# Performance work log

Measured on AMD Instinct MI355X. Metric: run time of the kernel, lower is better.

The kernel has to match this reference:

```python
import jax, jax.numpy as jnp
import numpy as np

B, S, D, H, M = 2, 2048, 1024, 16, 40
DH = D // H  # 64
L = S + M    # kv length after memory concat


def setup_inputs() -> dict:
    key = jax.random.key(0)
    ks = jax.random.split(key, 20)
    s = 1.0 / np.sqrt(D)
    inp = {
        'v': jax.random.normal(ks[0], (B, S, D), jnp.float32),
        'k': jax.random.normal(ks[1], (B, S, D), jnp.float32),
        'q': jax.random.normal(ks[2], (B, S, D), jnp.float32),
        # additive binary mask (1 = masked out), broadcast over heads
        'mask': jax.random.randint(ks[3], (B, 1, S, L), 0, 2).astype(jnp.float32),
        'Wq': jax.random.normal(ks[4], (D, D), jnp.float32) * s,
        'bq': jnp.zeros((D,), jnp.float32),
        'Wk': jax.random.normal(ks[5], (D, D), jnp.float32) * s,
        'bk': jnp.zeros((D,), jnp.float32),
        'Wv': jax.random.normal(ks[6], (D, D), jnp.float32) * s,
        'bv': jnp.zeros((D,), jnp.float32),
        'k_memory': jax.random.normal(ks[7], (1, M, D), jnp.float32) * (1.0 / np.sqrt(DH)),
        'v_memory': jax.random.normal(ks[8], (1, M, D), jnp.float32) * (1.0 / np.sqrt(M)),
        'Wkm': jax.random.normal(ks[9], (D, D), jnp.float32) * s,
        'bkm': jnp.zeros((D,), jnp.float32),
        'Wvm': jax.random.normal(ks[10], (D, D), jnp.float32) * s,
        'bvm': jnp.zeros((D,), jnp.float32),
        'Wo': jax.random.normal(ks[11], (D, D), jnp.float32) * s,
        'bo': jnp.zeros((D,), jnp.float32),
    }
    return inp


def _split_heads(x):
    # [B, T, D] -> [B, H, T, DH]
    b, t, _ = x.shape
    return x.reshape(b, t, H, DH).transpose(0, 2, 1, 3)


def reference(v, k, q, mask, Wq, bq, Wk, bk, Wv, bv, k_memory, v_memory,
              Wkm, bkm, Wvm, bvm, Wo, bo):
    qp = q @ Wq + bq
    kp = k @ Wk + bk
    vp = v @ Wv + bv
    km = (k_memory @ Wkm + bkm)  # [1, M, D]
    vm = (v_memory @ Wvm + bvm)  # [1, M, D]
    kc = jnp.concatenate([kp, jnp.broadcast_to(km, (kp.shape[0], M, D))], axis=1)
    vc = jnp.concatenate([vp, jnp.broadcast_to(vm, (vp.shape[0], M, D))], axis=1)
    qh, kh, vh = _split_heads(qp), _split_heads(kc), _split_heads(vc)
    # scores: [B, H, S, L]
    scores = jnp.einsum('bhqd,bhkd->bhqk', qh, kh) / np.sqrt(DH)
    scores = scores + mask * (-1e9)
    attn = jax.nn.softmax(scores, axis=-1)
    ctx = jnp.einsum('bhqk,bhkd->bhqd', attn, vh)  # [B, H, S, DH]
    ctx = ctx.transpose(0, 2, 1, 3).reshape(ctx.shape[0], S, D)
    out = ctx @ Wo + bo
    return (out, attn)
```

## Files before the change

### kernel.cpp

```cpp
#include <hip/hip_runtime.h>
#include <hip/hip_bf16.h>

typedef __attribute__((ext_vector_type(8))) short short8v;
typedef __attribute__((ext_vector_type(4))) short short4v;
typedef __attribute__((ext_vector_type(4))) float f32x4;

constexpr int B_ = 2, S_ = 2048, H_ = 16, MM_ = 40;
constexpr int L_ = S_ + MM_;
constexpr int LP_ = 2112;
constexpr int NT_ = 33;
constexpr float QSCALE = 0.18033688011112042f;

struct S2 { short hi, lo; };
__device__ __forceinline__ S2 split2(float f) {
    unsigned u = __builtin_bit_cast(unsigned, f);
    short hi = (short)(u >> 16);
    float fh = __builtin_bit_cast(float, u & 0xFFFF0000u);
    float fl = f - fh;
    short lo = (short)(__builtin_bit_cast(unsigned, fl) >> 16);
    return {hi, lo};
}
__device__ __forceinline__ short f2bh(float f) {
    unsigned u = __builtin_bit_cast(unsigned, f);
    u = (u + 0x7FFFu + ((u >> 16) & 1u)) >> 16;
    return (short)u;
}
__device__ __forceinline__ f32x4 mfma16(short8v a, short8v b, f32x4 c) {
    return __builtin_amdgcn_mfma_f32_16x16x32_bf16(a, b, c, 0, 0, 0);
}
__device__ __forceinline__ unsigned cvt_pk_bf16(float a, float b) {
    unsigned r;
    asm("v_cvt_pk_bf16_f32 %0, %1, %2" : "=v"(r) : "v"(a), "v"(b));
    return r;
}

__global__ __launch_bounds__(256) void wsplit6_kernel(
    const float* __restrict__ W0, const float* __restrict__ W1,
    const float* __restrict__ W2, const float* __restrict__ W3,
    const float* __restrict__ W4, const float* __restrict__ W5,
    short* __restrict__ WT)
{
    const float* Ws[6] = {W0, W1, W2, W3, W4, W5};
    const float* W = Ws[blockIdx.z];
    short* WTh = WT + (size_t)blockIdx.z * 2097152;
    short* WTl = WTh + 1048576;
    __shared__ float T[64][68];
    const int t = threadIdx.x;
    const int k0 = blockIdx.x * 64, n0 = blockIdx.y * 64;
    {
        int r = t >> 2, c = (t & 3) * 16;
        const float* src = W + (size_t)(k0 + r) * 1024 + n0 + c;
        *(float4*)&T[r][c + 0]  = *(const float4*)(src + 0);
        *(float4*)&T[r][c + 4]  = *(const float4*)(src + 4);
        *(float4*)&T[r][c + 8]  = *(const float4*)(src + 8);
        *(float4*)&T[r][c + 12] = *(const float4*)(src + 12);
    }
    __syncthreads();
    {
        int n = t >> 2, ks = (t & 3) * 16;
        short8v h0, h1, l0, l1;
#pragma unroll
        for (int j = 0; j < 8; ++j) {
            S2 a = split2(T[ks + j][n]);     h0[j] = a.hi; l0[j] = a.lo;
            S2 b = split2(T[ks + 8 + j][n]); h1[j] = b.hi; l1[j] = b.lo;
        }
        size_t dst = (size_t)(n0 + n) * 1024 + k0 + ks;
        *(short8v*)(WTh + dst) = h0;  *(short8v*)(WTh + dst + 8) = h1;
        *(short8v*)(WTl + dst) = l0;  *(short8v*)(WTl + dst + 8) = l1;
    }
}

__global__ __launch_bounds__(256) void pad_clear(short* __restrict__ Vh)
{
    int idx = blockIdx.x * 256 + threadIdx.x;
    if (idx >= 2048 * 24) return;
    int rd = idx / 24, l = L_ + idx % 24;
    Vh[(size_t)rd * LP_ + l] = 0;
}

template<int ASRC>
__device__ __forceinline__ void gemm_core(
    const float* __restrict__ Af, const short* __restrict__ Ahg,
    const short* __restrict__ Alg, const short* __restrict__ WTh,
    const short* __restrict__ WTl, const float* __restrict__ bias,
    float bscale, float scale,
    short* __restrict__ Oh, short* __restrict__ Ol, float* __restrict__ Of,
    int M, int RPB, int TD, int loff, int omode, int bx, int by,
    int kbeg, int kend)
{
    __shared__ short Ah[128][40];
    __shared__ short Al[128][40];
    __shared__ short Bh[128][40];
    __shared__ short Bl[128][40];
    const int tid = threadIdx.x;
    const int lane = tid & 63, wid = tid >> 6;
    const int wr = wid >> 1, wc = wid & 1;
    const int row0 = by * 128, col0 = bx * 128;
    const int sr = tid >> 1, sc = (tid & 1) << 4;

    f32x4 acc[4][4] = {};

    for (int k0 = kbeg; k0 < kend; k0 += 32) {
        if (ASRC == 0) {
            float f[16];
            int gr = row0 + sr;
            if (gr < M) {
                const float* ap = Af + (size_t)gr * 1024 + k0 + sc;
                float4 a0 = *(const float4*)(ap + 0);
                float4 a1 = *(const float4*)(ap + 4);
                float4 a2 = *(const float4*)(ap + 8);
                float4 a3 = *(const float4*)(ap + 12);
                f[0]=a0.x; f[1]=a0.y; f[2]=a0.z; f[3]=a0.w;
                f[4]=a1.x; f[5]=a1.y; f[6]=a1.z; f[7]=a1.w;
                f[8]=a2.x; f[9]=a2.y; f[10]=a2.z; f[11]=a2.w;
                f[12]=a3.x; f[13]=a3.y; f[14]=a3.z; f[15]=a3.w;
            } else {
#pragma unroll
                for (int j = 0; j < 16; ++j) f[j] = 0.f;
            }
            short8v h0, h1, l0, l1;
#pragma unroll
            for (int j = 0; j < 8; ++j) {
                S2 s = split2(f[j]); h0[j] = s.hi; l0[j] = s.lo;
            }
#pragma unroll
            for (int j = 0; j < 8; ++j) {
                S2 s = split2(f[8 + j]); h1[j] = s.hi; l1[j] = s.lo;
            }
            *(short8v*)&Ah[sr][sc] = h0; *(short8v*)&Ah[sr][sc + 8] = h1;
            *(short8v*)&Al[sr][sc] = l0; *(short8v*)&Al[sr][sc + 8] = l1;
        } else {
            const short* ah = Ahg + (size_t)(row0 + sr) * 1024 + k0 + sc;
            const short* al = Alg + (size_t)(row0 + sr) * 1024 + k0 + sc;
            *(short8v*)&Ah[sr][sc]     = *(const short8v*)ah;
            *(short8v*)&Ah[sr][sc + 8] = *(const short8v*)(ah + 8);
            *(short8v*)&Al[sr][sc]     = *(const short8v*)al;
            *(short8v*)&Al[sr][sc + 8] = *(const short8v*)(al + 8);
        }
        {
            const short* bh = WTh + (size_t)(col0 + sr) * 1024 + k0 + sc;
            const short* bl = WTl + (size_t)(col0 + sr) * 1024 + k0 + sc;
            *(short8v*)&Bh[sr][sc]     = *(const short8v*)bh;
            *(short8v*)&Bh[sr][sc + 8] = *(const short8v*)(bh + 8);
            *(short8v*)&Bl[sr][sc]     = *(const short8v*)bl;
            *(short8v*)&Bl[sr][sc + 8] = *(const short8v*)(bl + 8);
        }
        __syncthreads();
        const int kof = (lane >> 4) << 3;
        const int ar = lane & 15;
        short8v afh[4], afl[4], bfh[4], bfl[4];
#pragma unroll
        for (int i = 0; i < 4; ++i) {
            afh[i] = *(const short8v*)&Ah[wr * 64 + i * 16 + ar][kof];
            afl[i] = *(const short8v*)&Al[wr * 64 + i * 16 + ar][kof];
            bfh[i] = *(const short8v*)&Bh[wc * 64 + i * 16 + ar][kof];
            bfl[i] = *(const short8v*)&Bl[wc * 64 + i * 16 + ar][kof];
        }
#pragma unroll
        for (int i = 0; i < 4; ++i)
#pragma unroll
            for (int j = 0; j < 4; ++j) {
                acc[i][j] = mfma16(afh[i], bfh[j], acc[i][j]);
                acc[i][j] = mfma16(afh[i], bfl[j], acc[i][j]);
                acc[i][j] = mfma16(afl[i], bfh[j], acc[i][j]);
            }
        __syncthreads();
    }

#pragma unroll
    for (int i = 0; i < 4; ++i) {
#pragma unroll
        for (int j = 0; j < 4; ++j) {
            int colb = col0 + wc * 64 + j * 16 + (lane & 15);
            float bv = bias[colb] * bscale;
            int rowb = row0 + wr * 64 + i * 16 + ((lane >> 4) << 2);
            if (omode == 2) {
                if (rowb < M) {
                    int bb = rowb / RPB, tt = rowb % RPB;
                    int hh = colb >> 6, dh = colb & 63;
                    short4v hs;
#pragma unroll
                    for (int r = 0; r < 4; ++r)
                        hs[r] = f2bh((acc[i][j][r] + bv) * scale);
                    size_t dst = ((size_t)(bb * H_ + hh) * 64 + dh) * LP_ + loff + tt;
                    *(short4v*)(Oh + dst) = hs;
                }
            } else {
#pragma unroll
                for (int r = 0; r < 4; ++r) {
                    int row = rowb + r;
                    if (row < M) {
                        float o = (acc[i][j][r] + bv) * scale;
                        int bb = row / RPB, tt = row % RPB;
                        if (omode == 0) {
                            Of[((size_t)bb * TD + loff + tt) * 1024 + colb] = o;
                        } else {
                            int hh = colb >> 6, dh = colb & 63;
                            size_t dst = ((size_t)(bb * H_ + hh) * TD + loff + tt) * 64 + dh;
                            S2 s = split2(o);
                            Oh[dst] = s.hi; Ol[dst] = s.lo;
                        }
                    }
                }
            }
        }
    }
}

__global__ __launch_bounds__(256) void qkv_gemm(
    const float* __restrict__ q_in, const float* __restrict__ k_in,
    const float* __restrict__ v_in, const short* __restrict__ WT,
    const float* __restrict__ bq, const float* __restrict__ bk,
    const float* __restrict__ bv,
    short* __restrict__ Qh, short* __restrict__ Ql,
    short* __restrict__ Kh, short* __restrict__ Kl, short* __restrict__ Vh,
    const float* __restrict__ mask, unsigned* __restrict__ mp)
{
    const int z = blockIdx.z;
    if (z == 3) {
        const int blk = blockIdx.y * 8 + blockIdx.x;
        for (int rr = 0; rr < 16; ++rr) {
            const int row = blk * 16 + rr;
            const float* mr = mask + (size_t)row * L_;
            unsigned* orow = mp + (size_t)row * 68;
            for (int wd = threadIdx.x; wd < 66; wd += 256) {
                int l0 = wd * 32;
                unsigned bits = 0u;
                int lim = (wd < 65) ? 32 : 8;
                for (int j = 0; j < lim; j += 4) {
                    float4 m4 = *(const float4*)(mr + l0 + j);
                    bits |= ((unsigned)(m4.x != 0.f)) << (j + 0);
                    bits |= ((unsigned)(m4.y != 0.f)) << (j + 1);
                    bits |= ((unsigned)(m4.z != 0.f)) << (j + 2);
                    bits |= ((unsigned)(m4.w != 0.f)) << (j + 3);
                }
                if (wd == 65) bits |= 0xFFFFFF00u;
                orow[wd] = bits;
            }
        }
        return;
    }
    const float* A = (z == 0) ? q_in : (z == 1) ? k_in : v_in;
    const short* WTh = WT + (size_t)z * 2097152;
    const short* WTl = WTh + 1048576;
    const float* bias = (z == 0) ? bq : (z == 1) ? bk : bv;
    float scale = (z == 0) ? QSCALE : 1.0f;
    short* Oh = (z == 0) ? Qh : (z == 1) ? Kh : Vh;
    short* Ol = (z == 0) ? Ql : Kl;
    int omode = (z == 2) ? 2 : 1;
    int TD = (z == 0) ? S_ : LP_;
    gemm_core<0>(A, nullptr, nullptr, WTh, WTl, bias, 1.0f, scale,
                 Oh, Ol, nullptr, 4096, 2048, TD, 0, omode,
                 blockIdx.x, blockIdx.y, 0, 1024);
}

__global__ __launch_bounds__(256) void mem_gemm(
    const float* __restrict__ kmem, const float* __restrict__ vmem,
    const short* __restrict__ WT,
    const float* __restrict__ bkm, const float* __restrict__ bvm,
    short* __restrict__ Kh, short* __restrict__ Kl, short* __restrict__ Vh)
{
    const int z = blockIdx.z;
    const int which = z >> 1, b = z & 1;
    const float* A = which ? vmem : kmem;
    const short* WTh = WT + (size_t)(3 + which) * 2097152;
    const short* WTl = WTh + 1048576;
    const float* bias = which ? bvm : bkm;
    short* Oh = which ? (Vh + (size_t)b * H_ * 64 * LP_)
                      : (Kh + (size_t)b * H_ * LP_ * 64);
    short* Ol = which ? nullptr : (Kl + (size_t)b * H_ * LP_ * 64);
    gemm_core<0>(A, nullptr, nullptr, WTh, WTl, bias, 1.0f, 1.0f,
                 Oh, Ol, nullptr, 40, 40, LP_, S_, which ? 2 : 1,
                 blockIdx.x, blockIdx.y, 0, 1024);
}

__global__ __launch_bounds__(256) void out_gemm(
    const short* __restrict__ Ch, const short* __restrict__ Cl,
    const short* __restrict__ WT, const float* __restrict__ bo,
    float* __restrict__ Po0, float* __restrict__ Po1)
{
    const int z = blockIdx.z;
    const short* WTh = WT + (size_t)5 * 2097152;
    gemm_core<1>(nullptr, Ch, Cl, WTh, WTh + 1048576, bo,
                 z == 0 ? 1.0f : 0.0f, 1.0f,
                 nullptr, nullptr, z == 0 ? Po0 : Po1, 4096, 2048, S_, 0, 0,
                 blockIdx.x, blockIdx.y, z * 512, z * 512 + 512);
}

__global__ __launch_bounds__(256) void add_out(
    const float* __restrict__ Po0, const float* __restrict__ Po1,
    float* __restrict__ outp)
{
    int i = (blockIdx.x * 256 + threadIdx.x) * 4;
    float4 a = *(const float4*)(Po0 + i);
    float4 b = *(const float4*)(Po1 + i);
    a.x += b.x; a.y += b.y; a.z += b.z; a.w += b.w;
    *(float4*)(outp + i) = a;
}

__global__ __launch_bounds__(256) void attn4_kernel(
    const short* __restrict__ Qh, const short* __restrict__ Ql,
    const short* __restrict__ Kh, const short* __restrict__ Kl,
    const short* __restrict__ Vh, const unsigned* __restrict__ mp,
    float* __restrict__ attn, float* __restrict__ invg,
    short* __restrict__ Ch, short* __restrict__ Cl)
{
    __shared__ short KhB[2][64][64];
    __shared__ short KlB[2][64][64];
    __shared__ short VB[64][64];
    __shared__ short Ph[4][16][68];
    __shared__ float sbuf[4][16];

    const int id = blockIdx.x;
    const int wg = (id & 7) * 128 + (id >> 3);
    const int bh = wg >> 5, qb = wg & 31;
    const int b = bh >> 4, h = bh & 15;
    const int lane = threadIdx.x & 63, w = threadIdx.x >> 6;
    const int lq = lane & 15, hi = lane >> 4;
    const int sw = lq & 7;
    const int q0 = qb * 64 + w * 16;
    const int q = q0 + lq;

    const char* kh_g = (const char*)(Kh + (size_t)bh * LP_ * 64);
    const char* kl_g = (const char*)(Kl + (size_t)bh * LP_ * 64);
    const char* v_g  = (const char*)(Vh + (size_t)bh * 64 * LP_);

    auto stage_k = [&](int buf, int tt) {
#pragma unroll
        for (int i = 0; i < 2; ++i) {
            int o = w * 2048 + i * 1024 + lane * 16;
            int r = o >> 7, c = (o >> 4) & 7;
            int cs = c ^ (r & 7);
            const char* sh = kh_g + (size_t)tt * 8192 + r * 128 + cs * 16;
            const char* sl = kl_g + (size_t)tt * 8192 + r * 128 + cs * 16;
            __builtin_amdgcn_global_load_lds((const void*)sh,
                (void*)((char*)&KhB[buf][0][0] + w * 2048 + i * 1024), 16, 0, 0);
            __builtin_amdgcn_global_load_lds((const void*)sl,
                (void*)((char*)&KlB[buf][0][0] + w * 2048 + i * 1024), 16, 0, 0);
        }
    };
    auto stage_v = [&](int tt) {
#pragma unroll
        for (int i = 0; i < 2; ++i) {
            int o = w * 2048 + i * 1024 + lane * 16;
            int dh = o >> 7, c = (o >> 4) & 7;
            int cs = c ^ (dh & 7);
            const char* src = v_g + (size_t)dh * (LP_ * 2) + (size_t)tt * 128 + cs * 16;
            __builtin_amdgcn_global_load_lds((const void*)src,
                (void*)((char*)&VB[0][0] + w * 2048 + i * 1024), 16, 0, 0);
        }
    };

    const size_t qbase = ((size_t)bh * S_ + q) * 64 + hi * 8;
    const short8v qh0 = *(const short8v*)(Qh + qbase);
    const short8v qh1 = *(const short8v*)(Qh + qbase + 32);
    const short8v ql0 = *(const short8v*)(Ql + qbase);
    const short8v ql1 = *(const short8v*)(Ql + qbase + 32);
    const unsigned* mrow = mp + ((size_t)b * S_ + q) * 68;

    const int dr = lane >> 2, dc = lane & 3;
    short* dbase = (short*)(attn + ((size_t)bh * S_ + q0 + dr) * L_);

    float sm = 0.f;
    f32x4 pv[4] = {};

    stage_k(0, 0);
    stage_v(0);
    __syncthreads();

    int cur = 0;
    for (int t = 0; t < NT_; ++t) {
        if (t < NT_ - 1) stage_k(cur ^ 1, t + 1);

        const unsigned w0 = mrow[2 * t], w1 = mrow[2 * t + 1];
        const short8v* kp = (const short8v*)&KhB[cur][0][0];
        const short8v* lp = (const short8v*)&KlB[cur][0][0];
#pragma unroll
        for (int ls = 0; ls < 4; ++ls) {
            const int r = ls * 16 + lq;
            const short8v kh0 = kp[r * 8 + (hi ^ sw)];
            const short8v kh1 = kp[r * 8 + ((hi + 4) ^ sw)];
            const short8v kl0 = lp[r * 8 + (hi ^ sw)];
            const short8v kl1 = lp[r * 8 + ((hi + 4) ^ sw)];
            __builtin_amdgcn_s_setprio(1);
            f32x4 acc = {0.f, 0.f, 0.f, 0.f};
            acc = mfma16(kh0, qh0, acc); acc = mfma16(kh1, qh1, acc);
            acc = mfma16(kh0, ql0, acc); acc = mfma16(kh1, ql1, acc);
            acc = mfma16(kl0, qh0, acc); acc = mfma16(kl1, qh1, acc);
            __builtin_amdgcn_s_setprio(0);
            const unsigned wb = (ls & 2) ? w1 : w0;
            const int sh = (ls & 1) * 16 + hi * 4;
            float pr[4];
#pragma unroll
            for (int r2 = 0; r2 < 4; ++r2) {
                float e = __builtin_exp2f(acc[r2]);
                pr[r2] = ((wb >> (sh + r2)) & 1u) ? 0.f : e;
            }
            sm += (pr[0] + pr[1]) + (pr[2] + pr[3]);
            unsigned pk0 = cvt_pk_bf16(pr[0], pr[1]);
            unsigned pk1 = cvt_pk_bf16(pr[2], pr[3]);
            *(uint2*)&Ph[w][lq][ls * 16 + hi * 4] = uint2{pk0, pk1};
        }
        {
            short8v v0 = *(const short8v*)&Ph[w][dr][dc * 8];
            short8v v1 = *(const short8v*)&Ph[w][dr][32 + dc * 8];
            short* dst = dbase + t * 64 + dc * 8;
            if (t < NT_ - 1) {
                *(short8v*)dst = v0;
                *(short8v*)(dst + 32) = v1;
            } else {
                *(short8v*)dst = v0;
                if (dc == 0) *(short8v*)(dst + 32) = v1;
            }
        }
        __syncthreads();
        {
            const short8v pa0 = *(const short8v*)&Ph[w][lq][hi * 8];
            const short8v pa1 = *(const short8v*)&Ph[w][lq][32 + hi * 8];
            const short8v* vp = (const short8v*)&VB[0][0];
            __builtin_amdgcn_s_setprio(1);
#pragma unroll
            for (int j = 0; j < 4; ++j)
                pv[j] = mfma16(pa0, vp[(j * 16 + lq) * 8 + (hi ^ sw)], pv[j]);
#pragma unroll
            for (int j = 0; j < 4; ++j)
                pv[j] = mfma16(pa1, vp[(j * 16 + lq) * 8 + ((hi + 4) ^ sw)], pv[j]);
            __builtin_amdgcn_s_setprio(0);
        }
        __syncthreads();
        if (t < NT_ - 1) stage_v(t + 1);
        cur ^= 1;
    }

    sm += __shfl_xor(sm, 16);
    sm += __shfl_xor(sm, 32);
    if (lane < 16) sbuf[w][lane] = sm;
    __syncthreads();
    if (lane < 16) {
        float sv = sbuf[w][lane];
        invg[(size_t)bh * S_ + q0 + lane] = sv > 0.f ? 1.0f / sv : 0.f;
    }
    float iv[4];
#pragma unroll
    for (int r = 0; r < 4; ++r) {
        float sv = sbuf[w][hi * 4 + r];
        iv[r] = sv > 0.f ? 1.0f / sv : 0.f;
    }
#pragma unroll
    for (int j = 0; j < 4; ++j)
#pragma unroll
        for (int r = 0; r < 4; ++r) {
            float o = pv[j][r] * iv[r];
            size_t dst = ((size_t)b * S_ + q0 + hi * 4 + r) * 1024 + h * 64 + j * 16 + lq;
            S2 sp = split2(o);
            Ch[dst] = sp.hi; Cl[dst] = sp.lo;
        }
}

__global__ __launch_bounds__(256) void norm_attn(
    float* __restrict__ attn, const float* __restrict__ invg)
{
    __shared__ unsigned rowbuf[1044];
    const int row = blockIdx.x;
    const float iv = invg[row];
    float* rowp = attn + (size_t)row * L_;
    const unsigned* src = (const unsigned*)rowp;
    for (int i = threadIdx.x; i < 1044; i += 256) rowbuf[i] = src[i];
    __syncthreads();
    float4* dst = (float4*)rowp;
    for (int j = threadIdx.x; j < 522; j += 256) {
        unsigned u0 = rowbuf[2 * j], u1 = rowbuf[2 * j + 1];
        float4 v;
        v.x = __builtin_bit_cast(float, u0 << 16) * iv;
        v.y = __builtin_bit_cast(float, u0 & 0xFFFF0000u) * iv;
        v.z = __builtin_bit_cast(float, u1 << 16) * iv;
        v.w = __builtin_bit_cast(float, u1 & 0xFFFF0000u) * iv;
        dst[j] = v;
    }
}

extern "C" void kernel_launch(void* const* d_in, const int* in_sizes, int n_in,
                              void* d_out, int out_size, void* d_ws, size_t ws_size,
                              hipStream_t stream)
{
    const float* v_in = (const float*)d_in[0];
    const float* k_in = (const float*)d_in[1];
    const float* q_in = (const float*)d_in[2];
    const float* mask = (const float*)d_in[3];
    const float* Wq = (const float*)d_in[4];  const float* bq = (const float*)d_in[5];
    const float* Wk = (const float*)d_in[6];  const float* bk = (const float*)d_in[7];
    const float* Wv = (const float*)d_in[8];  const float* bv = (const float*)d_in[9];
    const float* kmem = (const float*)d_in[10];
    const float* vmem = (const float*)d_in[11];
    const float* Wkm = (const float*)d_in[12]; const float* bkm = (const float*)d_in[13];
    const float* Wvm = (const float*)d_in[14]; const float* bvm = (const float*)d_in[15];
    const float* Wo = (const float*)d_in[16];  const float* bo = (const float*)d_in[17];

    char* wsb = (char*)d_ws;
    short* WT  = (short*)(wsb);
    short* Qhb = (short*)(wsb + 25165824);
    short* Qlb = (short*)(wsb + 33554432);
    short* Khb = (short*)(wsb + 41943040);
    short* Klb = (short*)(wsb + 50593792);
    short* Vhb = (short*)(wsb + 59244544);
    short* Chb = (short*)(wsb + 67895296);
    short* Clb = (short*)(wsb + 76283904);
    float* invb = (float*)(wsb + 84672512);
    unsigned* mp = (unsigned*)(wsb + 84934656);
    if (ws_size < 86048768) return;
    float* Po0 = (float*)(wsb + 25165824);
    float* Po1 = (float*)(wsb + 41943040);

    float* outp = (float*)d_out;
    float* attnp = outp + (size_t)B_ * S_ * 1024;

    dim3 blk(256);

    wsplit6_kernel<<<dim3(16, 16, 6), blk, 0, stream>>>(Wq, Wk, Wv, Wkm, Wvm, Wo, WT);

    qkv_gemm<<<dim3(8, 32, 4), blk, 0, stream>>>(
        q_in, k_in, v_in, WT, bq, bk, bv, Qhb, Qlb, Khb, Klb, Vhb, mask, mp);

    mem_gemm<<<dim3(8, 1, 4), blk, 0, stream>>>(
        kmem, vmem, WT, bkm, bvm, Khb, Klb, Vhb);
    pad_clear<<<dim3(192), blk, 0, stream>>>(Vhb);

    attn4_kernel<<<dim3(1024), blk, 0, stream>>>(
        Qhb, Qlb, Khb, Klb, Vhb, mp, attnp, invb, Chb, Clb);

    out_gemm<<<dim3(8, 32, 2), blk, 0, stream>>>(Chb, Clb, WT, bo, Po0, Po1);
    add_out<<<dim3(4096), blk, 0, stream>>>(Po0, Po1, outp);

    norm_attn<<<dim3(B_ * H_ * S_), blk, 0, stream>>>(attnp, invb);
}
```

Before: 626.3 us.

## Fuse memory GEMM and pad clear into QKV launch, single-buffer attention K

Folds the memory-projection GEMM and V padding clear into the QKV GEMM launch as extra z-slices, which removes two kernel launches. The attention kernel drops K double-buffering: K and V for the next tile are staged together after the PV step, behind barriers on both sides, which reduces LDS use but exposes load latency. The row-sum reduction now uses shuffles instead of shared memory. The attention normalisation pass processes 32 rows per block with register loads instead of one row per block through LDS. The added z-slices with blockIdx.y != 0 exit immediately, so the grid includes idle blocks.

```diff
diff --git a/kernel.cpp b/kernel.cpp
--- a/kernel.cpp
+++ b/kernel.cpp
@@ -68,14 +68,6 @@
         *(short8v*)(WTh + dst) = h0;  *(short8v*)(WTh + dst + 8) = h1;
         *(short8v*)(WTl + dst) = l0;  *(short8v*)(WTl + dst + 8) = l1;
     }
-}
-
-__global__ __launch_bounds__(256) void pad_clear(short* __restrict__ Vh)
-{
-    int idx = blockIdx.x * 256 + threadIdx.x;
-    if (idx >= 2048 * 24) return;
-    int rd = idx / 24, l = L_ + idx % 24;
-    Vh[(size_t)rd * LP_ + l] = 0;
 }
 
 template<int ASRC>
@@ -209,15 +201,17 @@
 
 __global__ __launch_bounds__(256) void qkv_gemm(
     const float* __restrict__ q_in, const float* __restrict__ k_in,
-    const float* __restrict__ v_in, const short* __restrict__ WT,
+    const float* __restrict__ v_in, const float* __restrict__ kmem,
+    const float* __restrict__ vmem, const short* __restrict__ WT,
     const float* __restrict__ bq, const float* __restrict__ bk,
-    const float* __restrict__ bv,
+    const float* __restrict__ bv, const float* __restrict__ bkm,
+    const float* __restrict__ bvm,
     short* __restrict__ Qh, short* __restrict__ Ql,
     short* __restrict__ Kh, short* __restrict__ Kl, short* __restrict__ Vh,
     const float* __restrict__ mask, unsigned* __restrict__ mp)
 {
     const int z = blockIdx.z;
-    if (z == 3) {
+    if (z == 0) {
         const int blk = blockIdx.y * 8 + blockIdx.x;
         for (int rr = 0; rr < 16; ++rr) {
             const int row = blk * 16 + rr;
@@ -238,39 +232,40 @@
                 orow[wd] = bits;
             }
         }
+        for (int k = threadIdx.x; k < 192; k += 256) {
+            int g = blk * 192 + k;
+            int rd = g / 24, l = L_ + g % 24;
+            Vh[(size_t)rd * LP_ + l] = 0;
+        }
         return;
     }
-    const float* A = (z == 0) ? q_in : (z == 1) ? k_in : v_in;
-    const short* WTh = WT + (size_t)z * 2097152;
+    if (z >= 4) {
+        if (blockIdx.y != 0) return;
+        const int which = (z - 4) >> 1, b = (z - 4) & 1;
+        const float* A = which ? vmem : kmem;
+        const short* WTh = WT + (size_t)(3 + which) * 2097152;
+        const short* WTl = WTh + 1048576;
+        const float* bias = which ? bvm : bkm;
+        short* Oh = which ? (Vh + (size_t)b * H_ * 64 * LP_)
+                          : (Kh + (size_t)b * H_ * LP_ * 64);
+        short* Ol = which ? nullptr : (Kl + (size_t)b * H_ * LP_ * 64);
+        gemm_core<0>(A, nullptr, nullptr, WTh, WTl, bias, 1.0f, 1.0f,
+                     Oh, Ol, nullptr, 40, 40, LP_, S_, which ? 2 : 1,
+                     blockIdx.x, 0, 0, 1024);
+        return;
+    }
+    const int g = z - 1;
+    const float* A = (g == 0) ? q_in : (g == 1) ? k_in : v_in;
+    const short* WTh = WT + (size_t)g * 2097152;
     const short* WTl = WTh + 1048576;
-    const float* bias = (z == 0) ? bq : (z == 1) ? bk : bv;
-    float scale = (z == 0) ? QSCALE : 1.0f;
-    short* Oh = (z == 0) ? Qh : (z == 1) ? Kh : Vh;
-    short* Ol = (z == 0) ? Ql : Kl;
-    int omode = (z == 2) ? 2 : 1;
-    int TD = (z == 0) ? S_ : LP_;
+    const float* bias = (g == 0) ? bq : (g == 1) ? bk : bv;
+    float scale = (g == 0) ? QSCALE : 1.0f;
+    short* Oh = (g == 0) ? Qh : (g == 1) ? Kh : Vh;
+    short* Ol = (g == 0) ? Ql : Kl;
+    int omode = (g == 2) ? 2 : 1;
+    int TD = (g == 0) ? S_ : LP_;
     gemm_core<0>(A, nullptr, nullptr, WTh, WTl, bias, 1.0f, scale,
                  Oh, Ol, nullptr, 4096, 2048, TD, 0, omode,
-                 blockIdx.x, blockIdx.y, 0, 1024);
-}
-
-__global__ __launch_bounds__(256) void mem_gemm(
-    const float* __restrict__ kmem, const float* __restrict__ vmem,
-    const short* __restrict__ WT,
-    const float* __restrict__ bkm, const float* __restrict__ bvm,
-    short* __restrict__ Kh, short* __restrict__ Kl, short* __restrict__ Vh)
-{
-    const int z = blockIdx.z;
-    const int which = z >> 1, b = z & 1;
-    const float* A = which ? vmem : kmem;
-    const short* WTh = WT + (size_t)(3 + which) * 2097152;
-    const short* WTl = WTh + 1048576;
-    const float* bias = which ? bvm : bkm;
-    short* Oh = which ? (Vh + (size_t)b * H_ * 64 * LP_)
-                      : (Kh + (size_t)b * H_ * LP_ * 64);
-    short* Ol = which ? nullptr : (Kl + (size_t)b * H_ * LP_ * 64);
-    gemm_core<0>(A, nullptr, nullptr, WTh, WTl, bias, 1.0f, 1.0f,
-                 Oh, Ol, nullptr, 40, 40, LP_, S_, which ? 2 : 1,
                  blockIdx.x, blockIdx.y, 0, 1024);
 }
 
@@ -305,11 +300,10 @@
     float* __restrict__ attn, float* __restrict__ invg,
     short* __restrict__ Ch, short* __restrict__ Cl)
 {
-    __shared__ short KhB[2][64][64];
-    __shared__ short KlB[2][64][64];
+    __shared__ short KhB[64][64];
+    __shared__ short KlB[64][64];
     __shared__ short VB[64][64];
     __shared__ short Ph[4][16][68];
-    __shared__ float sbuf[4][16];
 
     const int id = blockIdx.x;
     const int wg = (id & 7) * 128 + (id >> 3);
@@ -325,7 +319,7 @@
     const char* kl_g = (const char*)(Kl + (size_t)bh * LP_ * 64);
     const char* v_g  = (const char*)(Vh + (size_t)bh * 64 * LP_);
 
-    auto stage_k = [&](int buf, int tt) {
+    auto stage_k = [&](int tt) {
 #pragma unroll
         for (int i = 0; i < 2; ++i) {
             int o = w * 2048 + i * 1024 + lane * 16;
@@ -334,9 +328,9 @@
             const char* sh = kh_g + (size_t)tt * 8192 + r * 128 + cs * 16;
             const char* sl = kl_g + (size_t)tt * 8192 + r * 128 + cs * 16;
             __builtin_amdgcn_global_load_lds((const void*)sh,
-                (void*)((char*)&KhB[buf][0][0] + w * 2048 + i * 1024), 16, 0, 0);
+                (void*)((char*)&KhB[0][0] + w * 2048 + i * 1024), 16, 0, 0);
             __builtin_amdgcn_global_load_lds((const void*)sl,
-                (void*)((char*)&KlB[buf][0][0] + w * 2048 + i * 1024), 16, 0, 0);
+                (void*)((char*)&KlB[0][0] + w * 2048 + i * 1024), 16, 0, 0);
         }
     };
     auto stage_v = [&](int tt) {
@@ -364,17 +358,14 @@
     float sm = 0.f;
     f32x4 pv[4] = {};
 
-    stage_k(0, 0);
+    stage_k(0);
     stage_v(0);
     __syncthreads();
 
-    int cur = 0;
     for (int t = 0; t < NT_; ++t) {
-        if (t < NT_ - 1) stage_k(cur ^ 1, t + 1);
-
         const unsigned w0 = mrow[2 * t], w1 = mrow[2 * t + 1];
-        const short8v* kp = (const short8v*)&KhB[cur][0][0];
-        const short8v* lp = (const short8v*)&KlB[cur][0][0];
+        const short8v* kp = (const short8v*)&KhB[0][0];
+        const short8v* lp = (const short8v*)&KlB[0][0];
 #pragma unroll
         for (int ls = 0; ls < 4; ++ls) {
             const int r = ls * 16 + lq;
@@ -397,23 +388,16 @@
                 pr[r2] = ((wb >> (sh + r2)) & 1u) ? 0.f : e;
             }
             sm += (pr[0] + pr[1]) + (pr[2] + pr[3]);
-            unsigned pk0 = cvt_pk_bf16(pr[0], pr[1]);
-            unsigned pk1 = cvt_pk_bf16(pr[2], pr[3]);
-            *(uint2*)&Ph[w][lq][ls * 16 + hi * 4] = uint2{pk0, pk1};
+            *(uint2*)&Ph[w][lq][ls * 16 + hi * 4] =
+                uint2{cvt_pk_bf16(pr[0], pr[1]), cvt_pk_bf16(pr[2], pr[3])};
         }
         {
             short8v v0 = *(const short8v*)&Ph[w][dr][dc * 8];
             short8v v1 = *(const short8v*)&Ph[w][dr][32 + dc * 8];
             short* dst = dbase + t * 64 + dc * 8;
-            if (t < NT_ - 1) {
-                *(short8v*)dst = v0;
-                *(short8v*)(dst + 32) = v1;
-            } else {
-                *(short8v*)dst = v0;
-                if (dc == 0) *(short8v*)(dst + 32) = v1;
-            }
-        }
-        __syncthreads();
+            if (t < NT_ - 1) { *(short8v*)dst = v0; *(short8v*)(dst + 32) = v1; }
+            else { *(short8v*)dst = v0; if (dc == 0) *(short8v*)(dst + 32) = v1; }
+        }
         {
             const short8v pa0 = *(const short8v*)&Ph[w][lq][hi * 8];
             const short8v pa1 = *(const short8v*)&Ph[w][lq][32 + hi * 8];
@@ -427,55 +411,63 @@
                 pv[j] = mfma16(pa1, vp[(j * 16 + lq) * 8 + ((hi + 4) ^ sw)], pv[j]);
             __builtin_amdgcn_s_setprio(0);
         }
-        __syncthreads();
-        if (t < NT_ - 1) stage_v(t + 1);
-        cur ^= 1;
+        if (t < NT_ - 1) {
+            __syncthreads();
+            stage_k(t + 1);
+            stage_v(t + 1);
+            __syncthreads();
+        }
     }
 
     sm += __shfl_xor(sm, 16);
     sm += __shfl_xor(sm, 32);
-    if (lane < 16) sbuf[w][lane] = sm;
-    __syncthreads();
-    if (lane < 16) {
-        float sv = sbuf[w][lane];
-        invg[(size_t)bh * S_ + q0 + lane] = sv > 0.f ? 1.0f / sv : 0.f;
-    }
-    float iv[4];
+    if (lane < 16)
+        invg[(size_t)bh * S_ + q0 + lane] = sm > 0.f ? 1.0f / sm : 0.f;
+
 #pragma unroll
     for (int r = 0; r < 4; ++r) {
-        float sv = sbuf[w][hi * 4 + r];
-        iv[r] = sv > 0.f ? 1.0f / sv : 0.f;
-    }
-#pragma unroll
-    for (int j = 0; j < 4; ++j)
-#pragma unroll
-        for (int r = 0; r < 4; ++r) {
-            float o = pv[j][r] * iv[r];
+        float sv = __shfl(sm, hi * 4 + r);
+        float iv = sv > 0.f ? 1.0f / sv : 0.f;
+#pragma unroll
+        for (int j = 0; j < 4; ++j) {
             size_t dst = ((size_t)b * S_ + q0 + hi * 4 + r) * 1024 + h * 64 + j * 16 + lq;
-            S2 sp = split2(o);
+            S2 sp = split2(pv[j][r] * iv);
             Ch[dst] = sp.hi; Cl[dst] = sp.lo;
         }
+    }
 }
 
 __global__ __launch_bounds__(256) void norm_attn(
     float* __restrict__ attn, const float* __restrict__ invg)
 {
-    __shared__ unsigned rowbuf[1044];
-    const int row = blockIdx.x;
-    const float iv = invg[row];
-    float* rowp = attn + (size_t)row * L_;
-    const unsigned* src = (const unsigned*)rowp;
-    for (int i = threadIdx.x; i < 1044; i += 256) rowbuf[i] = src[i];
-    __syncthreads();
-    float4* dst = (float4*)rowp;
-    for (int j = threadIdx.x; j < 522; j += 256) {
-        unsigned u0 = rowbuf[2 * j], u1 = rowbuf[2 * j + 1];
-        float4 v;
-        v.x = __builtin_bit_cast(float, u0 << 16) * iv;
-        v.y = __builtin_bit_cast(float, u0 & 0xFFFF0000u) * iv;
-        v.z = __builtin_bit_cast(float, u1 << 16) * iv;
-        v.w = __builtin_bit_cast(float, u1 & 0xFFFF0000u) * iv;
-        dst[j] = v;
+    const int nb = blockIdx.x;
+    const int lane = threadIdx.x & 63, w = threadIdx.x >> 6;
+#pragma unroll 1
+    for (int i = 0; i < 8; ++i) {
+        const int row = nb * 32 + w * 8 + i;
+        const float iv = invg[row];
+        float* rowf = attn + (size_t)row * L_;
+        unsigned* rw = (unsigned*)rowf;
+        unsigned u[17];
+#pragma unroll
+        for (int it = 0; it < 16; ++it) u[it] = rw[lane + it * 64];
+        if (lane < 20) u[16] = rw[lane + 1024];
+        asm volatile("s_waitcnt vmcnt(0)" ::: "memory");
+#pragma unroll
+        for (int it = 0; it < 16; ++it) {
+            unsigned uu = u[it];
+            float2 v;
+            v.x = __builtin_bit_cast(float, uu << 16) * iv;
+            v.y = __builtin_bit_cast(float, uu & 0xFFFF0000u) * iv;
+            *(float2*)(rowf + 2 * (lane + it * 64)) = v;
+        }
+        if (lane < 20) {
+            unsigned uu = u[16];
+            float2 v;
+            v.x = __builtin_bit_cast(float, uu << 16) * iv;
+            v.y = __builtin_bit_cast(float, uu & 0xFFFF0000u) * iv;
+            *(float2*)(rowf + 2 * (lane + 1024)) = v;
+        }
     }
 }
 
@@ -518,12 +510,9 @@
 
     wsplit6_kernel<<<dim3(16, 16, 6), blk, 0, stream>>>(Wq, Wk, Wv, Wkm, Wvm, Wo, WT);
 
-    qkv_gemm<<<dim3(8, 32, 4), blk, 0, stream>>>(
-        q_in, k_in, v_in, WT, bq, bk, bv, Qhb, Qlb, Khb, Klb, Vhb, mask, mp);
-
-    mem_gemm<<<dim3(8, 1, 4), blk, 0, stream>>>(
-        kmem, vmem, WT, bkm, bvm, Khb, Klb, Vhb);
-    pad_clear<<<dim3(192), blk, 0, stream>>>(Vhb);
+    qkv_gemm<<<dim3(8, 32, 8), blk, 0, stream>>>(
+        q_in, k_in, v_in, kmem, vmem, WT, bq, bk, bv, bkm, bvm,
+        Qhb, Qlb, Khb, Klb, Vhb, mask, mp);
 
     attn4_kernel<<<dim3(1024), blk, 0, stream>>>(
         Qhb, Qlb, Khb, Klb, Vhb, mp, attnp, invb, Chb, Clb);
@@ -531,5 +520,5 @@
     out_gemm<<<dim3(8, 32, 2), blk, 0, stream>>>(Chb, Clb, WT, bo, Po0, Po1);
     add_out<<<dim3(4096), blk, 0, stream>>>(Po0, Po1, outp);
 
-    norm_attn<<<dim3(B_ * H_ * S_), blk, 0, stream>>>(attnp, invb);
-}
+    norm_attn<<<dim3(2048), blk, 0, stream>>>(attnp, invb);
+}
```

After: 570.0 us, median of 2. 1.1x faster.
